# Kernel optimization log

Hardware: AMD Instinct MI355X
Metric: run time of the kernel (lower is better)

## Reference

```python
import jax, jax.numpy as jnp
import numpy as np

EPS = 1e-6
BASE_CURVATURE = 1.0


def _artanh(x):
    return jnp.arctanh(jnp.clip(x, -1.0 + 1e-5, 1.0 - 1e-5))


def _norm(x):
    return jnp.maximum(jnp.linalg.norm(x, axis=-1, keepdims=True), EPS)


def _logmap0(x, c):
    # Poincare-ball log map at origin
    sc = jnp.sqrt(c)
    n = _norm(x)
    return _artanh(sc * n) * x / (sc * n)


def _expmap0(v, c):
    # Poincare-ball exp map at origin
    sc = jnp.sqrt(c)
    n = _norm(v)
    return jnp.tanh(sc * n) * v / (sc * n)


def _mobius_add(x, y, c):
    x2 = jnp.sum(x * x, axis=-1, keepdims=True)
    y2 = jnp.sum(y * y, axis=-1, keepdims=True)
    xy = jnp.sum(x * y, axis=-1, keepdims=True)
    num = (1.0 + 2.0 * c * xy + c * y2) * x + (1.0 - c * x2) * y
    den = 1.0 + 2.0 * c * xy + (c * c) * x2 * y2
    return num / jnp.maximum(den, EPS)


def _mobius_scalar_mul(t, x, c):
    sc = jnp.sqrt(c)
    n = _norm(x)
    return jnp.tanh(t * _artanh(sc * n)) * x / (sc * n)


def setup_inputs() -> dict:
    key = jax.random.key(0)
    ks = jax.random.split(key, 8)
    B, D_in, D_out, K = 4096, 2048, 2048, 4
    scale_w = np.sqrt(2.0 / (D_in + D_out)) * 0.1
    return {
        "x": jax.random.normal(ks[0], (B, D_in), jnp.float32) * 0.05,
        "weight": jax.random.normal(ks[1], (D_out, D_in), jnp.float32) * scale_w,
        "bias": jax.random.normal(ks[2], (D_out,), jnp.float32) * 0.01,
        "curv_weight": jax.random.normal(ks[3], (1, D_in), jnp.float32) * 0.1,
        "curv_bias": jnp.zeros((1,), jnp.float32),
        "anchors": jax.random.normal(ks[4], (K, D_out), jnp.float32) * 0.3,
        "t_values": jnp.full((K,), 0.5, jnp.float32),
        "anchor_weights": jnp.full((K,), 1.0 / K, jnp.float32),
    }


def reference(x, weight, bias, curv_weight, curv_bias, anchors, t_values, anchor_weights):
    # 1) dynamic curvature prediction: c_i = base_c * softplus(x . w + b), then mean
    logits = x @ curv_weight[0] + curv_bias[0]                 # [B]
    curvatures = BASE_CURVATURE * jax.nn.softplus(logits)      # [B]
    c = jax.lax.stop_gradient(jnp.mean(curvatures))            # scalar (.item() in torch)

    # 2) fused hyperbolic linear: expmap0(logmap0(x) @ W^T + b)
    u = _logmap0(x, c)                                         # [B, D_in]
    h = u @ weight.T + bias                                    # [B, D_out]
    y = _expmap0(h, c)                                         # [B, D_out]

    # 3) geodesic activation: weighted Mobius geodesic toward each anchor
    xe = y[:, None, :]                                         # [B, 1, D]
    a = anchors[None, :, :]                                    # [1, K, D]
    diff = _mobius_add(-xe, a, c)                              # [B, K, D]
    step = _mobius_scalar_mul(t_values[None, :, None], diff, c)
    g = _mobius_add(xe, step, c)                               # [B, K, D]
    w = jax.nn.softmax(anchor_weights)                         # [K]
    return jnp.einsum("bkd,k->bd", g, w)                       # [B, D_out]
```

## Files before the change

kernel.cpp:

```cpp
#include <hip/hip_runtime.h>
#include <stdint.h>

#define B_ROWS 4096
#define D_IN   2048
#define D_OUT  2048
#define KANCH  4

typedef _Float16 half8  __attribute__((ext_vector_type(8)));
typedef _Float16 half4  __attribute__((ext_vector_type(4)));
typedef float    floatx4 __attribute__((ext_vector_type(4)));
typedef const __attribute__((address_space(1))) uint8_t* gptr_t;
typedef __attribute__((address_space(3))) uint8_t* lptr_t;

__global__ __launch_bounds__(256) void k_convw(
    const float* __restrict__ W, _Float16* __restrict__ Wh)
{
    int idx = blockIdx.x * 256 + threadIdx.x;
    const floatx4* W4 = (const floatx4*)W;
    floatx4 v = W4[idx];
    half4 h = {(_Float16)v[0], (_Float16)v[1], (_Float16)v[2], (_Float16)v[3]};
    *(half4*)(Wh + (size_t)idx * 4) = h;
}

__global__ __launch_bounds__(256) void k_convx_rowstats(
    const float* __restrict__ x,
    const float* __restrict__ cw,
    const float* __restrict__ cb,
    _Float16* __restrict__ xh,
    float* __restrict__ n2x, float* __restrict__ sprow)
{
    int w = threadIdx.x >> 6, lane = threadIdx.x & 63;
    int row = blockIdx.x * 4 + w;
    const floatx4* xr = (const floatx4*)(x + (size_t)row * D_IN);
    const floatx4* wr = (const floatx4*)cw;
    _Float16* xo = xh + (size_t)row * D_IN;
    float dot = 0.f, ss = 0.f;
#pragma unroll
    for (int i = 0; i < 8; ++i) {
        int idx = i * 64 + lane;
        floatx4 xv = xr[idx];
        floatx4 wv = wr[idx];
#pragma unroll
        for (int j = 0; j < 4; ++j) {
            dot += xv[j] * wv[j];
            ss  += xv[j] * xv[j];
        }
        half4 h = {(_Float16)xv[0], (_Float16)xv[1], (_Float16)xv[2], (_Float16)xv[3]};
        *(half4*)(xo + idx * 4) = h;
    }
#pragma unroll
    for (int off = 32; off; off >>= 1) {
        dot += __shfl_down(dot, off);
        ss  += __shfl_down(ss, off);
    }
    if (lane == 0) {
        n2x[row] = ss;
        float z = dot + cb[0];
        sprow[row] = (z > 20.f) ? z : log1pf(expf(z));
    }
}

__global__ __launch_bounds__(256) void k_finalize(
    const float* __restrict__ anchors,
    const float* __restrict__ n2x,
    const float* __restrict__ sprow,
    float* __restrict__ frow,
    float* __restrict__ scal)
{
    int tid = threadIdx.x, w = tid >> 6, lane = tid & 63;
    __shared__ float spw[4];
    __shared__ float s_c;
    float sp = 0.f;
#pragma unroll
    for (int i = 0; i < 16; ++i) sp += sprow[tid + 256 * i];
#pragma unroll
    for (int off = 32; off; off >>= 1) sp += __shfl_down(sp, off);
    if (lane == 0) spw[w] = sp;
    const floatx4* ar = (const floatx4*)(anchors + (size_t)w * D_OUT);
    float aa = 0.f;
#pragma unroll
    for (int i = 0; i < 8; ++i) {
        floatx4 av = ar[i * 64 + lane];
#pragma unroll
        for (int j = 0; j < 4; ++j) aa += av[j] * av[j];
    }
#pragma unroll
    for (int off = 32; off; off >>= 1) aa += __shfl_down(aa, off);
    if (lane == 0) scal[2 + w] = aa;
    __syncthreads();
    if (tid == 0) {
        float c = (spw[0] + spw[1] + spw[2] + spw[3]) * (1.0f / (float)B_ROWS);
        scal[1] = c;
        s_c = c;
    }
    __syncthreads();
    float sc = sqrtf(s_c);
    for (int b = tid; b < B_ROWS; b += 256) {
        float n = fmaxf(sqrtf(n2x[b]), 1e-6f);
        float a = sc * n;
        float zc = fminf(fmaxf(a, -1.0f + 1e-5f), 1.0f - 1e-5f);
        frow[b] = atanhf(zc) / a;
    }
}

__global__ __launch_bounds__(256) void k_gemm(
    const _Float16* __restrict__ A,
    const _Float16* __restrict__ W,
    const float* __restrict__ bias,
    const float* __restrict__ frow,
    float* __restrict__ H)
{
    constexpr int K = D_IN;
    __shared__ __align__(16) _Float16 As[128 * 64];
    __shared__ __align__(16) _Float16 Bs[128 * 64];
    int tid = threadIdx.x;
    int lane = tid & 63;
    int w = tid >> 6;
    int wm = (w >> 1) * 64, wn = (w & 1) * 64;
    int bm0 = blockIdx.y * 128, bn0 = blockIdx.x * 128;

    floatx4 acc[4][4];
#pragma unroll
    for (int mi = 0; mi < 4; ++mi)
#pragma unroll
        for (int ni = 0; ni < 4; ++ni)
            acc[mi][ni] = (floatx4){0.f, 0.f, 0.f, 0.f};

    for (int k0 = 0; k0 < K; k0 += 64) {
#pragma unroll
        for (int i = 0; i < 4; ++i) {
            int e = (i * 256 + tid) * 8;
            int r = e >> 6, kk = e & 63;
            __builtin_amdgcn_global_load_lds(
                (gptr_t)(A + (size_t)(bm0 + r) * K + k0 + kk),
                (lptr_t)(As + e), 16, 0, 0);
            __builtin_amdgcn_global_load_lds(
                (gptr_t)(W + (size_t)(bn0 + r) * K + k0 + kk),
                (lptr_t)(Bs + e), 16, 0, 0);
        }
        __syncthreads();
#pragma unroll
        for (int ks = 0; ks < 64; ks += 32) {
            int kq = ks + (lane >> 4) * 8;
            half8 afr[4], bfr[4];
#pragma unroll
            for (int mi = 0; mi < 4; ++mi)
                afr[mi] = *(const half8*)(As + (wm + mi * 16 + (lane & 15)) * 64 + kq);
#pragma unroll
            for (int ni = 0; ni < 4; ++ni)
                bfr[ni] = *(const half8*)(Bs + (wn + ni * 16 + (lane & 15)) * 64 + kq);
#pragma unroll
            for (int mi = 0; mi < 4; ++mi)
#pragma unroll
                for (int ni = 0; ni < 4; ++ni)
                    acc[mi][ni] = __builtin_amdgcn_mfma_f32_16x16x32_f16(
                        afr[mi], bfr[ni], acc[mi][ni], 0, 0, 0);
        }
        __syncthreads();
    }
#pragma unroll
    for (int mi = 0; mi < 4; ++mi) {
#pragma unroll
        for (int r = 0; r < 4; ++r) {
            int gm = bm0 + wm + mi * 16 + (lane >> 4) * 4 + r;
            float f = frow[gm];
#pragma unroll
            for (int ni = 0; ni < 4; ++ni) {
                int gn = bn0 + wn + ni * 16 + (lane & 15);
                H[(size_t)gm * D_OUT + gn] = f * acc[mi][ni][r] + bias[gn];
            }
        }
    }
}

__global__ __launch_bounds__(256) void k_mobius(
    const float* __restrict__ anchors,
    const float* __restrict__ tv,
    const float* __restrict__ aw,
    const float* __restrict__ scal,
    float* __restrict__ out)
{
    int tid = threadIdx.x, w = tid >> 6, lane = tid & 63;
    size_t rowoff = (size_t)blockIdx.x * D_OUT;
    float hf[8];
    *(floatx4*)(hf)     = *(const floatx4*)(out + rowoff + tid * 8);
    *(floatx4*)(hf + 4) = *(const floatx4*)(out + rowoff + tid * 8 + 4);
    float af[KANCH][8];
#pragma unroll
    for (int k = 0; k < KANCH; ++k) {
        *(floatx4*)(af[k])     = *(const floatx4*)(anchors + (size_t)k * D_OUT + tid * 8);
        *(floatx4*)(af[k] + 4) = *(const floatx4*)(anchors + (size_t)k * D_OUT + tid * 8 + 4);
    }
    float v[5] = {0.f, 0.f, 0.f, 0.f, 0.f};
#pragma unroll
    for (int j = 0; j < 8; ++j) {
        v[0] += hf[j] * hf[j];
#pragma unroll
        for (int k = 0; k < KANCH; ++k) v[1 + k] += hf[j] * af[k][j];
    }
#pragma unroll
    for (int off = 32; off; off >>= 1)
#pragma unroll
        for (int q = 0; q < 5; ++q) v[q] += __shfl_down(v[q], off);
    __shared__ float red[4][5];
    if (lane == 0)
#pragma unroll
        for (int q = 0; q < 5; ++q) red[w][q] = v[q];
    __syncthreads();
    __shared__ float coef[1 + KANCH];
    if (tid == 0) {
        float hh = red[0][0] + red[1][0] + red[2][0] + red[3][0];
        float ha[KANCH];
        for (int k = 0; k < KANCH; ++k)
            ha[k] = red[0][1 + k] + red[1][1 + k] + red[2][1 + k] + red[3][1 + k];
        float c = scal[1], sc = sqrtf(c);
        float mx = -1e30f;
        for (int k = 0; k < KANCH; ++k) mx = fmaxf(mx, aw[k]);
        float se = 0.f, wk[KANCH];
        for (int k = 0; k < KANCH; ++k) { wk[k] = expf(aw[k] - mx); se += wk[k]; }
        for (int k = 0; k < KANCH; ++k) wk[k] /= se;
        float nh = fmaxf(sqrtf(hh), 1e-6f);
        float snh = sc * nh;
        float gy = tanhf(snh) / snh;
        float x2 = gy * gy * hh;
        float B1 = 1.f - c * x2;
        float ch = 0.f;
        for (int k = 0; k < KANCH; ++k) {
            float y2 = scal[2 + k];
            float dy = gy * ha[k];
            float xy1 = -dy;
            float A1 = 1.f + 2.f * c * xy1 + c * y2;
            float den1 = fmaxf(1.f + 2.f * c * xy1 + c * c * x2 * y2, 1e-6f);
            float al = -A1 / den1, be = B1 / den1;
            float nd2 = fmaxf(al * al * x2 + 2.f * al * be * dy + be * be * y2, 0.f);
            float nd = fmaxf(sqrtf(nd2), 1e-6f);
            float snd = sc * nd;
            float zc = fminf(fmaxf(snd, -1.f + 1e-5f), 1.f - 1e-5f);
            float s = tanhf(tv[k] * atanhf(zc)) / snd;
            float y2s = s * s * nd2;
            float xys = s * (al * x2 + be * dy);
            float A2 = 1.f + 2.f * c * xys + c * y2s;
            float den2 = fmaxf(1.f + 2.f * c * xys + c * c * x2 * y2s, 1e-6f);
            float Cy  = (A2 + B1 * s * al) / den2;
            float Cak = (B1 * s * be) / den2;
            ch += wk[k] * Cy;
            coef[1 + k] = wk[k] * Cak;
        }
        coef[0] = gy * ch;
    }
    __syncthreads();
    float Ch = coef[0];
    float o[8];
#pragma unroll
    for (int j = 0; j < 8; ++j) {
        float val = Ch * hf[j];
#pragma unroll
        for (int k = 0; k < KANCH; ++k) val += coef[1 + k] * af[k][j];
        o[j] = val;
    }
    *(floatx4*)(out + rowoff + tid * 8)     = *(floatx4*)(o);
    *(floatx4*)(out + rowoff + tid * 8 + 4) = *(floatx4*)(o + 4);
}

extern "C" void kernel_launch(void* const* d_in, const int* in_sizes, int n_in,
                              void* d_out, int out_size, void* d_ws, size_t ws_size,
                              hipStream_t stream) {
    const float* x       = (const float*)d_in[0];
    const float* wt      = (const float*)d_in[1];
    const float* bias    = (const float*)d_in[2];
    const float* cw      = (const float*)d_in[3];
    const float* cb      = (const float*)d_in[4];
    const float* anchors = (const float*)d_in[5];
    const float* tv      = (const float*)d_in[6];
    const float* aw      = (const float*)d_in[7];
    float* out = (float*)d_out;

    _Float16* Wh = (_Float16*)d_ws;
    _Float16* xh = Wh + (size_t)D_OUT * D_IN;
    float* fws   = (float*)(xh + (size_t)B_ROWS * D_IN);
    float* n2x   = fws;
    float* sprow = n2x + B_ROWS;
    float* frow  = sprow + B_ROWS;
    float* scal  = frow + B_ROWS;

    k_convw<<<(D_OUT * D_IN) / (256 * 4), 256, 0, stream>>>(wt, Wh);
    k_convx_rowstats<<<B_ROWS / 4, 256, 0, stream>>>(x, cw, cb, xh, n2x, sprow);
    k_finalize<<<1, 256, 0, stream>>>(anchors, n2x, sprow, frow, scal);
    k_gemm<<<dim3(D_OUT / 128, B_ROWS / 128), 256, 0, stream>>>(xh, Wh, bias, frow, out);
    k_mobius<<<B_ROWS, 256, 0, stream>>>(anchors, tv, aw, scal, out);
}
```

Before: 193.7 us.

## Merge prep kernels, split-K GEMM, and fold row scaling and bias into mobius

```diff
diff --git a/kernel.cpp b/kernel.cpp
--- a/kernel.cpp
+++ b/kernel.cpp
@@ -12,105 +12,71 @@
 typedef const __attribute__((address_space(1))) uint8_t* gptr_t;
 typedef __attribute__((address_space(3))) uint8_t* lptr_t;
 
-__global__ __launch_bounds__(256) void k_convw(
-    const float* __restrict__ W, _Float16* __restrict__ Wh)
-{
-    int idx = blockIdx.x * 256 + threadIdx.x;
-    const floatx4* W4 = (const floatx4*)W;
-    floatx4 v = W4[idx];
-    half4 h = {(_Float16)v[0], (_Float16)v[1], (_Float16)v[2], (_Float16)v[3]};
-    *(half4*)(Wh + (size_t)idx * 4) = h;
-}
-
-__global__ __launch_bounds__(256) void k_convx_rowstats(
+__global__ __launch_bounds__(256) void k_prep(
     const float* __restrict__ x,
+    const float* __restrict__ W,
     const float* __restrict__ cw,
     const float* __restrict__ cb,
     _Float16* __restrict__ xh,
-    float* __restrict__ n2x, float* __restrict__ sprow)
-{
-    int w = threadIdx.x >> 6, lane = threadIdx.x & 63;
-    int row = blockIdx.x * 4 + w;
-    const floatx4* xr = (const floatx4*)(x + (size_t)row * D_IN);
-    const floatx4* wr = (const floatx4*)cw;
-    _Float16* xo = xh + (size_t)row * D_IN;
-    float dot = 0.f, ss = 0.f;
-#pragma unroll
-    for (int i = 0; i < 8; ++i) {
-        int idx = i * 64 + lane;
-        floatx4 xv = xr[idx];
-        floatx4 wv = wr[idx];
-#pragma unroll
-        for (int j = 0; j < 4; ++j) {
-            dot += xv[j] * wv[j];
-            ss  += xv[j] * xv[j];
-        }
-        half4 h = {(_Float16)xv[0], (_Float16)xv[1], (_Float16)xv[2], (_Float16)xv[3]};
-        *(half4*)(xo + idx * 4) = h;
-    }
-#pragma unroll
-    for (int off = 32; off; off >>= 1) {
-        dot += __shfl_down(dot, off);
-        ss  += __shfl_down(ss, off);
-    }
-    if (lane == 0) {
-        n2x[row] = ss;
-        float z = dot + cb[0];
-        sprow[row] = (z > 20.f) ? z : log1pf(expf(z));
-    }
-}
-
-__global__ __launch_bounds__(256) void k_finalize(
-    const float* __restrict__ anchors,
-    const float* __restrict__ n2x,
-    const float* __restrict__ sprow,
-    float* __restrict__ frow,
+    _Float16* __restrict__ Wh,
+    float* __restrict__ n2x,
     float* __restrict__ scal)
 {
-    int tid = threadIdx.x, w = tid >> 6, lane = tid & 63;
-    __shared__ float spw[4];
-    __shared__ float s_c;
-    float sp = 0.f;
-#pragma unroll
-    for (int i = 0; i < 16; ++i) sp += sprow[tid + 256 * i];
-#pragma unroll
-    for (int off = 32; off; off >>= 1) sp += __shfl_down(sp, off);
-    if (lane == 0) spw[w] = sp;
-    const floatx4* ar = (const floatx4*)(anchors + (size_t)w * D_OUT);
-    float aa = 0.f;
-#pragma unroll
-    for (int i = 0; i < 8; ++i) {
-        floatx4 av = ar[i * 64 + lane];
-#pragma unroll
-        for (int j = 0; j < 4; ++j) aa += av[j] * av[j];
-    }
-#pragma unroll
-    for (int off = 32; off; off >>= 1) aa += __shfl_down(aa, off);
-    if (lane == 0) scal[2 + w] = aa;
-    __syncthreads();
-    if (tid == 0) {
-        float c = (spw[0] + spw[1] + spw[2] + spw[3]) * (1.0f / (float)B_ROWS);
-        scal[1] = c;
-        s_c = c;
-    }
-    __syncthreads();
-    float sc = sqrtf(s_c);
-    for (int b = tid; b < B_ROWS; b += 256) {
-        float n = fmaxf(sqrtf(n2x[b]), 1e-6f);
-        float a = sc * n;
-        float zc = fminf(fmaxf(a, -1.0f + 1e-5f), 1.0f - 1e-5f);
-        frow[b] = atanhf(zc) / a;
-    }
-}
-
-__global__ __launch_bounds__(256) void k_gemm(
+    int tid = threadIdx.x;
+    if (blockIdx.x < 1024) {
+        int w = tid >> 6, lane = tid & 63;
+        int row = blockIdx.x * 4 + w;
+        const floatx4* xr = (const floatx4*)(x + (size_t)row * D_IN);
+        const floatx4* wr = (const floatx4*)cw;
+        _Float16* xo = xh + (size_t)row * D_IN;
+        float dot = 0.f, ss = 0.f;
+#pragma unroll
+        for (int i = 0; i < 8; ++i) {
+            int idx = i * 64 + lane;
+            floatx4 xv = xr[idx];
+            floatx4 wv = wr[idx];
+#pragma unroll
+            for (int j = 0; j < 4; ++j) {
+                dot += xv[j] * wv[j];
+                ss  += xv[j] * xv[j];
+            }
+            half4 h = {(_Float16)xv[0], (_Float16)xv[1], (_Float16)xv[2], (_Float16)xv[3]};
+            *(half4*)(xo + idx * 4) = h;
+        }
+#pragma unroll
+        for (int off = 32; off; off >>= 1) {
+            dot += __shfl_down(dot, off);
+            ss  += __shfl_down(ss, off);
+        }
+        __shared__ float spw[4];
+        if (lane == 0) {
+            n2x[row] = ss;
+            float z = dot + cb[0];
+            spw[w] = (z > 20.f) ? z : log1pf(expf(z));
+        }
+        __syncthreads();
+        if (tid == 0)
+            atomicAdd(&scal[0], spw[0] + spw[1] + spw[2] + spw[3]);
+    } else {
+        int blk = blockIdx.x - 1024;
+        const floatx4* W4 = (const floatx4*)W;
+#pragma unroll
+        for (int i = 0; i < 4; ++i) {
+            int idx = blk * 1024 + i * 256 + tid;
+            floatx4 v = W4[idx];
+            half4 h = {(_Float16)v[0], (_Float16)v[1], (_Float16)v[2], (_Float16)v[3]};
+            *(half4*)(Wh + (size_t)idx * 4) = h;
+        }
+    }
+}
+
+template<int KPB>
+__global__ __launch_bounds__(256, 4) void k_gemm(
     const _Float16* __restrict__ A,
     const _Float16* __restrict__ W,
-    const float* __restrict__ bias,
-    const float* __restrict__ frow,
-    float* __restrict__ H)
+    float* __restrict__ P0,
+    float* __restrict__ P1)
 {
-    constexpr int K = D_IN;
     __shared__ __align__(16) _Float16 As[128 * 64];
     __shared__ __align__(16) _Float16 Bs[128 * 64];
     int tid = threadIdx.x;
@@ -118,6 +84,8 @@
     int w = tid >> 6;
     int wm = (w >> 1) * 64, wn = (w & 1) * 64;
     int bm0 = blockIdx.y * 128, bn0 = blockIdx.x * 128;
+    float* P = (blockIdx.z == 0) ? P0 : P1;
+    int kbase = blockIdx.z * KPB;
 
     floatx4 acc[4][4];
 #pragma unroll
@@ -126,16 +94,16 @@
         for (int ni = 0; ni < 4; ++ni)
             acc[mi][ni] = (floatx4){0.f, 0.f, 0.f, 0.f};
 
-    for (int k0 = 0; k0 < K; k0 += 64) {
+    for (int k0 = 0; k0 < KPB; k0 += 64) {
 #pragma unroll
         for (int i = 0; i < 4; ++i) {
             int e = (i * 256 + tid) * 8;
             int r = e >> 6, kk = e & 63;
             __builtin_amdgcn_global_load_lds(
-                (gptr_t)(A + (size_t)(bm0 + r) * K + k0 + kk),
+                (gptr_t)(A + (size_t)(bm0 + r) * D_IN + kbase + k0 + kk),
                 (lptr_t)(As + e), 16, 0, 0);
             __builtin_amdgcn_global_load_lds(
-                (gptr_t)(W + (size_t)(bn0 + r) * K + k0 + kk),
+                (gptr_t)(W + (size_t)(bn0 + r) * D_IN + kbase + k0 + kk),
                 (lptr_t)(Bs + e), 16, 0, 0);
         }
         __syncthreads();
@@ -163,57 +131,84 @@
 #pragma unroll
         for (int r = 0; r < 4; ++r) {
             int gm = bm0 + wm + mi * 16 + (lane >> 4) * 4 + r;
-            float f = frow[gm];
 #pragma unroll
             for (int ni = 0; ni < 4; ++ni) {
                 int gn = bn0 + wn + ni * 16 + (lane & 15);
-                H[(size_t)gm * D_OUT + gn] = f * acc[mi][ni][r] + bias[gn];
+                P[(size_t)gm * D_OUT + gn] = acc[mi][ni][r];
             }
         }
     }
 }
 
 __global__ __launch_bounds__(256) void k_mobius(
+    const float* __restrict__ P1,
+    const float* __restrict__ bias,
     const float* __restrict__ anchors,
     const float* __restrict__ tv,
     const float* __restrict__ aw,
+    const float* __restrict__ n2x,
     const float* __restrict__ scal,
+    int split,
     float* __restrict__ out)
 {
     int tid = threadIdx.x, w = tid >> 6, lane = tid & 63;
     size_t rowoff = (size_t)blockIdx.x * D_OUT;
-    float hf[8];
-    *(floatx4*)(hf)     = *(const floatx4*)(out + rowoff + tid * 8);
-    *(floatx4*)(hf + 4) = *(const floatx4*)(out + rowoff + tid * 8 + 4);
+    float pf[8], bf[8];
+    *(floatx4*)(pf)     = *(const floatx4*)(out + rowoff + tid * 8);
+    *(floatx4*)(pf + 4) = *(const floatx4*)(out + rowoff + tid * 8 + 4);
+    if (split == 2) {
+        floatx4 q0 = *(const floatx4*)(P1 + rowoff + tid * 8);
+        floatx4 q1 = *(const floatx4*)(P1 + rowoff + tid * 8 + 4);
+#pragma unroll
+        for (int j = 0; j < 4; ++j) { pf[j] += q0[j]; pf[4 + j] += q1[j]; }
+    }
+    *(floatx4*)(bf)     = *(const floatx4*)(bias + tid * 8);
+    *(floatx4*)(bf + 4) = *(const floatx4*)(bias + tid * 8 + 4);
     float af[KANCH][8];
 #pragma unroll
     for (int k = 0; k < KANCH; ++k) {
         *(floatx4*)(af[k])     = *(const floatx4*)(anchors + (size_t)k * D_OUT + tid * 8);
         *(floatx4*)(af[k] + 4) = *(const floatx4*)(anchors + (size_t)k * D_OUT + tid * 8 + 4);
     }
-    float v[5] = {0.f, 0.f, 0.f, 0.f, 0.f};
+    float v[15];
+#pragma unroll
+    for (int q = 0; q < 15; ++q) v[q] = 0.f;
 #pragma unroll
     for (int j = 0; j < 8; ++j) {
-        v[0] += hf[j] * hf[j];
-#pragma unroll
-        for (int k = 0; k < KANCH; ++k) v[1 + k] += hf[j] * af[k][j];
+        v[0] += pf[j] * pf[j];
+        v[1] += pf[j] * bf[j];
+        v[6] += bf[j] * bf[j];
+#pragma unroll
+        for (int k = 0; k < KANCH; ++k) {
+            v[2 + k]  += pf[j] * af[k][j];
+            v[7 + k]  += bf[j] * af[k][j];
+            v[11 + k] += af[k][j] * af[k][j];
+        }
     }
 #pragma unroll
     for (int off = 32; off; off >>= 1)
 #pragma unroll
-        for (int q = 0; q < 5; ++q) v[q] += __shfl_down(v[q], off);
-    __shared__ float red[4][5];
+        for (int q = 0; q < 15; ++q) v[q] += __shfl_down(v[q], off);
+    __shared__ float red[4][15];
     if (lane == 0)
 #pragma unroll
-        for (int q = 0; q < 5; ++q) red[w][q] = v[q];
+        for (int q = 0; q < 15; ++q) red[w][q] = v[q];
     __syncthreads();
-    __shared__ float coef[1 + KANCH];
+    __shared__ float cf[2 + KANCH];
     if (tid == 0) {
-        float hh = red[0][0] + red[1][0] + red[2][0] + red[3][0];
+        float t[15];
+#pragma unroll
+        for (int q = 0; q < 15; ++q)
+            t[q] = red[0][q] + red[1][q] + red[2][q] + red[3][q];
+        float c = scal[0] * (1.0f / (float)B_ROWS);
+        float sc = sqrtf(c);
+        float nx = fmaxf(sqrtf(n2x[blockIdx.x]), 1e-6f);
+        float ax = sc * nx;
+        float zx = fminf(fmaxf(ax, -1.f + 1e-5f), 1.f - 1e-5f);
+        float f = atanhf(zx) / ax;
+        float hh = f * f * t[0] + 2.f * f * t[1] + t[6];
         float ha[KANCH];
-        for (int k = 0; k < KANCH; ++k)
-            ha[k] = red[0][1 + k] + red[1][1 + k] + red[2][1 + k] + red[3][1 + k];
-        float c = scal[1], sc = sqrtf(c);
+        for (int k = 0; k < KANCH; ++k) ha[k] = f * t[2 + k] + t[7 + k];
         float mx = -1e30f;
         for (int k = 0; k < KANCH; ++k) mx = fmaxf(mx, aw[k]);
         float se = 0.f, wk[KANCH];
@@ -226,7 +221,7 @@
         float B1 = 1.f - c * x2;
         float ch = 0.f;
         for (int k = 0; k < KANCH; ++k) {
-            float y2 = scal[2 + k];
+            float y2 = t[11 + k];
             float dy = gy * ha[k];
             float xy1 = -dy;
             float A1 = 1.f + 2.f * c * xy1 + c * y2;
@@ -244,18 +239,20 @@
             float Cy  = (A2 + B1 * s * al) / den2;
             float Cak = (B1 * s * be) / den2;
             ch += wk[k] * Cy;
-            coef[1 + k] = wk[k] * Cak;
-        }
-        coef[0] = gy * ch;
+            cf[2 + k] = wk[k] * Cak;
+        }
+        float c0 = gy * ch;
+        cf[0] = c0 * f;
+        cf[1] = c0;
     }
     __syncthreads();
-    float Ch = coef[0];
+    float cp = cf[0], cb_ = cf[1];
     float o[8];
 #pragma unroll
     for (int j = 0; j < 8; ++j) {
-        float val = Ch * hf[j];
-#pragma unroll
-        for (int k = 0; k < KANCH; ++k) val += coef[1 + k] * af[k][j];
+        float val = cp * pf[j] + cb_ * bf[j];
+#pragma unroll
+        for (int k = 0; k < KANCH; ++k) val += cf[2 + k] * af[k][j];
         o[j] = val;
     }
     *(floatx4*)(out + rowoff + tid * 8)     = *(floatx4*)(o);
@@ -277,15 +274,17 @@
 
     _Float16* Wh = (_Float16*)d_ws;
     _Float16* xh = Wh + (size_t)D_OUT * D_IN;
-    float* fws   = (float*)(xh + (size_t)B_ROWS * D_IN);
-    float* n2x   = fws;
-    float* sprow = n2x + B_ROWS;
-    float* frow  = sprow + B_ROWS;
-    float* scal  = frow + B_ROWS;
-
-    k_convw<<<(D_OUT * D_IN) / (256 * 4), 256, 0, stream>>>(wt, Wh);
-    k_convx_rowstats<<<B_ROWS / 4, 256, 0, stream>>>(x, cw, cb, xh, n2x, sprow);
-    k_finalize<<<1, 256, 0, stream>>>(anchors, n2x, sprow, frow, scal);
-    k_gemm<<<dim3(D_OUT / 128, B_ROWS / 128), 256, 0, stream>>>(xh, Wh, bias, frow, out);
-    k_mobius<<<B_ROWS, 256, 0, stream>>>(anchors, tv, aw, scal, out);
-}
+    float* n2x   = (float*)(xh + (size_t)B_ROWS * D_IN);
+    float* scal  = n2x + B_ROWS;
+    float* P1    = scal + 8;
+    size_t need_split = (size_t)((char*)(P1 + (size_t)B_ROWS * D_OUT) - (char*)d_ws);
+    int split = (ws_size >= need_split) ? 2 : 1;
+
+    hipMemsetAsync(scal, 0, sizeof(float), stream);
+    k_prep<<<2048, 256, 0, stream>>>(x, wt, cw, cb, xh, Wh, n2x, scal);
+    if (split == 2)
+        k_gemm<D_IN / 2><<<dim3(D_OUT / 128, B_ROWS / 128, 2), 256, 0, stream>>>(xh, Wh, out, P1);
+    else
+        k_gemm<D_IN><<<dim3(D_OUT / 128, B_ROWS / 128, 1), 256, 0, stream>>>(xh, Wh, out, P1);
+    k_mobius<<<B_ROWS, 256, 0, stream>>>(P1, bias, anchors, tv, aw, n2x, scal, split, out);
+}
```

Measured after the change: 207.5 us. +7.1%, slower.
